# Kernel optimization log

Measured on AMD Instinct MI355X. Metric: run time of the kernel, lower is better.

Reference implementation:

```python
import jax, jax.numpy as jnp
import numpy as np
import math

DIM = 1024
WINDOW = 16
NUM_HEADS = 16
HEAD_DIM = DIM // NUM_HEADS
SCALE = math.sqrt(HEAD_DIM)
LN_EPS = 1e-5


def _gather_window(z, W):
    # z: [B, T, H, C] -> [B, T, H, W, C]; nb[:, t, :, w, :] = z[:, t-1-w] (zeros if t-1-w < 0)
    B, T, H, C = z.shape
    t = jnp.arange(T)[:, None]
    w = jnp.arange(W)[None, :]
    idx = t - 1 - w                      # [T, W]
    valid = idx >= 0
    idxc = jnp.clip(idx, 0, T - 1)
    nb = z[:, idxc]                      # [B, T, W, H, C]
    nb = jnp.where(valid[None, :, :, None, None], nb, jnp.zeros((), z.dtype))
    return nb.transpose(0, 1, 3, 2, 4)   # [B, T, H, W, C]


def setup_inputs() -> dict:
    key = jax.random.key(0)
    k0, k1, k2, k3 = jax.random.split(key, 4)
    B, T, D = 2, 4096, DIM
    x = jax.random.normal(k0, (B, T, D), dtype=jnp.float32)
    wq = jax.random.normal(k1, (D, D), dtype=jnp.float32) * 0.02
    wkv = jax.random.normal(k2, (2 * D, D), dtype=jnp.float32) * 0.02  # torch Linear weight layout [out,in]
    wo = jax.random.normal(k3, (D, D), dtype=jnp.float32) * 0.02
    gamma = jnp.ones((D,), dtype=jnp.float32)
    beta = jnp.zeros((D,), dtype=jnp.float32)
    return {"x": x, "wq": wq, "wkv": wkv, "wo": wo, "gamma": gamma, "beta": beta}


def reference(x, wq, wkv, wo, gamma, beta):
    B, T, D = x.shape
    H, HD, W = NUM_HEADS, HEAD_DIM, WINDOW
    q = (x @ wq.T).reshape(B, T, H, HD)
    kv = (x @ wkv.T).reshape(B, T, H, 2 * HD)
    nb_kv = _gather_window(kv, W)                    # [B, T, H, W, 2*HD]
    nb_k, nb_v = nb_kv[..., :HD], nb_kv[..., HD:]
    tau = jax.nn.sigmoid(jnp.einsum('bthd,bthwd->bthw', q, nb_k) / SCALE)
    msg = jnp.einsum('bthw,bthwd->bthd', tau, nb_v)  # [B, T, H, HD]
    y = x + msg.reshape(B, T, D) @ wo.T
    mu = jnp.mean(y, axis=-1, keepdims=True)
    var = jnp.mean((y - mu) ** 2, axis=-1, keepdims=True)
    out = (y - mu) * jax.lax.rsqrt(var + LN_EPS) * gamma + beta
    return out
```

## Files before the change

### kernel.cpp

```cpp
#include <hip/hip_runtime.h>
#include <hip/hip_bf16.h>

#define D_MODEL 1024
#define SEQ_T   4096
#define NBATCH  2
#define NHEADS  16
#define HEAD_D  64
#define WIN     16

typedef __attribute__((ext_vector_type(8))) short bf16x8;
typedef __attribute__((ext_vector_type(8))) unsigned short u16x8;
typedef __attribute__((ext_vector_type(4))) float f32x4;

__device__ __forceinline__ unsigned short f2bf(float f) {
  union { float f; unsigned int u; } v; v.f = f;
  unsigned int r = v.u + 0x7fffu + ((v.u >> 16) & 1u);
  return (unsigned short)(r >> 16);
}
__device__ __forceinline__ float bf2f(unsigned short u) {
  union { unsigned int u; float f; } v; v.u = ((unsigned int)u) << 16;
  return v.f;
}

#define SBAR() __builtin_amdgcn_s_barrier()
#define LGKM0() asm volatile("s_waitcnt lgkmcnt(0)" ::: "memory")
#define LGKM8() asm volatile("s_waitcnt lgkmcnt(8)" ::: "memory")
#define VMC(n) asm volatile("s_waitcnt vmcnt(" #n ")" ::: "memory")

__global__ __launch_bounds__(256) void cast_f32_bf16(const float4* __restrict__ src,
                                                     ushort* __restrict__ dst, int n4) {
  int i = blockIdx.x * 256 + threadIdx.x;
  if (i >= n4) return;
  float4 v = src[i];
  ushort4 o;
  o.x = f2bf(v.x); o.y = f2bf(v.y); o.z = f2bf(v.z); o.w = f2bf(v.w);
  *(ushort4*)(dst + (size_t)i * 4) = o;
}

__global__ __launch_bounds__(256) void cast_weights(const float4* __restrict__ wq,
                                                    const float4* __restrict__ wkv,
                                                    const float4* __restrict__ wo,
                                                    ushort* __restrict__ dst) {
  int i = blockIdx.x * 256 + threadIdx.x;
  const float4* src;
  int off;
  if (i < 262144) { src = wq; off = 0; }
  else if (i < 786432) { src = wkv; off = 262144; }
  else { src = wo; off = 786432; }
  float4 v = src[i - off];
  ushort4 o;
  o.x = f2bf(v.x); o.y = f2bf(v.y); o.z = f2bf(v.z); o.w = f2bf(v.w);
  *(ushort4*)(dst + (size_t)i * 4) = o;
}

__global__ __launch_bounds__(512, 2) void gemm1_6ph(const ushort* __restrict__ A,
                                                    const ushort* __restrict__ Bt,
                                                    ushort* __restrict__ C,
                                                    int M, int N, int K) {
  extern __shared__ char smem[];
  const int tid = threadIdx.x;
  const int wid = tid >> 6;
  const int lane = tid & 63;
  const int m0 = blockIdx.y * 256;
  const int n0 = blockIdx.x * 192;

  const int l8 = lane >> 3;
  const int lchunk = (lane & 7) ^ (l8 & 7);
  const ushort* pA = A + (size_t)(m0 + wid * 8 + l8) * K + lchunk * 8;
  const ushort* pB = Bt + (size_t)(n0 + wid * 8 + l8) * K + lchunk * 8;

#define SA(kt, db, j0)                                                                     \
  {                                                                                        \
    _Pragma("unroll") for (int j = (j0); j < (j0) + 2; ++j) {                              \
      const ushort* gp = pA + (size_t)(j * 64) * K + (size_t)(kt) * 64;                    \
      char* lp = smem + (db) * 32768 + (j * 8 + wid) * 1024;                               \
      __builtin_amdgcn_global_load_lds((const __attribute__((address_space(1))) void*)gp,  \
                                       (__attribute__((address_space(3))) void*)lp, 16, 0, 0); \
    }                                                                                      \
  }
#define SB(kt, db)                                                                         \
  {                                                                                        \
    _Pragma("unroll") for (int j = 0; j < 3; ++j) {                                        \
      const ushort* gp = pB + (size_t)(j * 64) * K + (size_t)(kt) * 64;                    \
      char* lp = smem + 65536 + (db) * 24576 + (j * 8 + wid) * 1024;                       \
      __builtin_amdgcn_global_load_lds((const __attribute__((address_space(1))) void*)gp,  \
                                       (__attribute__((address_space(3))) void*)lp, 16, 0, 0); \
    }                                                                                      \
  }

  const int fr = lane & 15;
  const int g = lane >> 4;
  const int wr = wid >> 1;
  const int wc = wid & 1;
  int aRow[4], bRow[6], ch[2];
#pragma unroll
  for (int mi = 0; mi < 4; ++mi) aRow[mi] = (wr * 64 + mi * 16 + fr) * 128;
#pragma unroll
  for (int j = 0; j < 6; ++j) bRow[j] = (wc * 96 + j * 16 + fr) * 128;
#pragma unroll
  for (int kk = 0; kk < 2; ++kk) ch[kk] = ((kk * 4 + g) ^ (fr & 7)) * 16;

  f32x4 acc[4][6];
#pragma unroll
  for (int mi = 0; mi < 4; ++mi)
#pragma unroll
    for (int j = 0; j < 6; ++j) acc[mi][j] = (f32x4){0.f, 0.f, 0.f, 0.f};

  bf16x8 a[4][2], b[2][2];

#define RD_A(db)                                                               \
  _Pragma("unroll") for (int mi = 0; mi < 4; ++mi)                             \
    _Pragma("unroll") for (int kk = 0; kk < 2; ++kk)                           \
      a[mi][kk] = *(const bf16x8*)(smem + (db) * 32768 + aRow[mi] + ch[kk]);
#define RD_B(db, nh)                                                           \
  _Pragma("unroll") for (int ni = 0; ni < 2; ++ni)                             \
    _Pragma("unroll") for (int kk = 0; kk < 2; ++kk)                           \
      b[ni][kk] = *(const bf16x8*)(smem + 65536 + (db) * 24576 +               \
                                   bRow[(nh) * 2 + ni] + ch[kk]);
#define MM(nh)                                                                 \
  __builtin_amdgcn_s_setprio(1);                                               \
  _Pragma("unroll") for (int kk = 0; kk < 2; ++kk)                             \
    _Pragma("unroll") for (int mi = 0; mi < 4; ++mi)                           \
      _Pragma("unroll") for (int ni = 0; ni < 2; ++ni)                         \
        acc[mi][(nh) * 2 + ni] = __builtin_amdgcn_mfma_f32_16x16x32_bf16(      \
            a[mi][kk], b[ni][kk], acc[mi][(nh) * 2 + ni], 0, 0, 0);            \
  __builtin_amdgcn_s_setprio(0);

  SA(0, 0, 0); SA(0, 0, 2); SB(0, 0); SA(1, 1, 0); SA(1, 1, 2);
  VMC(4);
  SBAR();

#pragma unroll 1
  for (int i = 0; i < 8; ++i) {
    const int t1 = 2 * i + 1;
    const int t2 = (2 * i + 2 < 16) ? 2 * i + 2 : 15;
    const int t3 = (2 * i + 3 < 16) ? 2 * i + 3 : 15;
    const int d2 = t2 & 1, d3 = t3 & 1;

    RD_A(0); RD_B(0, 0);
    SB(t1, 1);
    LGKM8();
    SBAR(); LGKM0();
    MM(0);
    SBAR();

    RD_B(0, 1);
    SA(t2, d2, 0);
    SBAR(); LGKM0();
    MM(1);
    SBAR();

    RD_B(0, 2);
    SA(t2, d2, 2);
    VMC(4);
    SBAR(); LGKM0();
    MM(2);
    SBAR();

    RD_A(1); RD_B(1, 0);
    SB(t2, d2);
    LGKM8();
    SBAR(); LGKM0();
    MM(0);
    SBAR();

    RD_B(1, 1);
    SA(t3, d3, 0);
    SBAR(); LGKM0();
    MM(1);
    SBAR();

    RD_B(1, 2);
    SA(t3, d3, 2);
    VMC(4);
    SBAR(); LGKM0();
    MM(2);
    SBAR();
  }

  const int cc = lane & 15;
  const int cr4 = (lane >> 4) * 4;
#pragma unroll
  for (int mi = 0; mi < 4; ++mi)
#pragma unroll
    for (int j = 0; j < 6; ++j)
#pragma unroll
      for (int r = 0; r < 4; ++r) {
        int row = m0 + wr * 64 + mi * 16 + cr4 + r;
        int col = n0 + wc * 96 + j * 16 + cc;
        C[(size_t)row * N + col] = f2bf(acc[mi][j][r]);
      }
#undef SA
#undef SB
#undef RD_A
#undef RD_B
#undef MM
}

template <int EPI>
__global__ __launch_bounds__(512, 2) void gemm_8w(const ushort* __restrict__ A,
                                                  const ushort* __restrict__ Bt,
                                                  ushort* __restrict__ Cb,
                                                  float* __restrict__ Cf,
                                                  const float* __restrict__ resid,
                                                  int M, int N, int K) {
  extern __shared__ char smem[];
  const int NTK = K >> 6;
  const int tid = threadIdx.x;
  const int wid = tid >> 6;
  const int lane = tid & 63;
  const int m0 = blockIdx.y * 256;
  const int n0 = blockIdx.x * 128;

  const int l8 = lane >> 3;
  const int lchunk = (lane & 7) ^ (l8 & 7);
  const ushort* pA = A + (size_t)(m0 + wid * 8 + l8) * K + lchunk * 8;
  const ushort* pB = Bt + (size_t)(n0 + wid * 8 + l8) * K + lchunk * 8;

#define STAGE_A(kt, db)                                                                    \
  {                                                                                        \
    _Pragma("unroll") for (int j = 0; j < 4; ++j) {                                        \
      const ushort* gp = pA + (size_t)(j * 64) * K + (size_t)(kt) * 64;                    \
      char* lp = smem + (db) * 32768 + (j * 8 + wid) * 1024;                               \
      __builtin_amdgcn_global_load_lds((const __attribute__((address_space(1))) void*)gp,  \
                                       (__attribute__((address_space(3))) void*)lp, 16, 0, 0); \
    }                                                                                      \
  }
#define STAGE_B(kt, db)                                                                    \
  {                                                                                        \
    _Pragma("unroll") for (int j = 0; j < 2; ++j) {                                        \
      const ushort* gp = pB + (size_t)(j * 64) * K + (size_t)(kt) * 64;                    \
      char* lp = smem + 65536 + (db) * 16384 + (j * 8 + wid) * 1024;                       \
      __builtin_amdgcn_global_load_lds((const __attribute__((address_space(1))) void*)gp,  \
                                       (__attribute__((address_space(3))) void*)lp, 16, 0, 0); \
    }                                                                                      \
  }

  const int fr = lane & 15;
  const int g = lane >> 4;
  const int wr = wid >> 1;
  const int wc = wid & 1;
  int aRow[4], bRow[2][2], ch[2];
#pragma unroll
  for (int mi = 0; mi < 4; ++mi) aRow[mi] = (wr * 64 + mi * 16 + fr) * 128;
#pragma unroll
  for (int nq = 0; nq < 2; ++nq)
#pragma unroll
    for (int ni = 0; ni < 2; ++ni) bRow[nq][ni] = (wc * 64 + nq * 32 + ni * 16 + fr) * 128;
#pragma unroll
  for (int kk = 0; kk < 2; ++kk) ch[kk] = ((kk * 4 + g) ^ (fr & 7)) * 16;

  f32x4 acc[2][4][2];
#pragma unroll
  for (int nq = 0; nq < 2; ++nq)
#pragma unroll
    for (int mi = 0; mi < 4; ++mi)
#pragma unroll
      for (int ni = 0; ni < 2; ++ni) acc[nq][mi][ni] = (f32x4){0.f, 0.f, 0.f, 0.f};

  bf16x8 a[4][2], b0[2][2], b1[2][2];

  STAGE_A(0, 0); STAGE_B(0, 0); STAGE_A(1, 1);
  VMC(4);
  SBAR();

#define PHASE_MFMA(nq, bfr)                                                    \
  __builtin_amdgcn_s_setprio(1);                                               \
  _Pragma("unroll") for (int kk = 0; kk < 2; ++kk)                             \
    _Pragma("unroll") for (int mi = 0; mi < 4; ++mi)                           \
      _Pragma("unroll") for (int ni = 0; ni < 2; ++ni)                         \
        acc[nq][mi][ni] = __builtin_amdgcn_mfma_f32_16x16x32_bf16(             \
            a[mi][kk], bfr[ni][kk], acc[nq][mi][ni], 0, 0, 0);                 \
  __builtin_amdgcn_s_setprio(0);

#pragma unroll 1
  for (int t = 0; t < NTK; ++t) {
    const int db = t & 1;
    const int u1 = (t + 1 < NTK) ? t + 1 : NTK - 1;
    const int u2 = (t + 2 < NTK) ? t + 2 : NTK - 1;
    const int d1 = u1 & 1, d2 = u2 & 1;
    const char* Ab = smem + db * 32768;
    const char* Bb = smem + 65536 + db * 16384;

#pragma unroll
    for (int mi = 0; mi < 4; ++mi)
#pragma unroll
      for (int kk = 0; kk < 2; ++kk)
        a[mi][kk] = *(const bf16x8*)(Ab + aRow[mi] + ch[kk]);
#pragma unroll
    for (int ni = 0; ni < 2; ++ni)
#pragma unroll
      for (int kk = 0; kk < 2; ++kk)
        b0[ni][kk] = *(const bf16x8*)(Bb + bRow[0][ni] + ch[kk]);
    STAGE_B(u1, d1);
    LGKM0();
    PHASE_MFMA(0, b0);
    VMC(2);
    SBAR();

#pragma unroll
    for (int ni = 0; ni < 2; ++ni)
#pragma unroll
      for (int kk = 0; kk < 2; ++kk)
        b1[ni][kk] = *(const bf16x8*)(Bb + bRow[1][ni] + ch[kk]);
    STAGE_A(u2, d2);
    LGKM0();
    PHASE_MFMA(1, b1);
    VMC(4);
    SBAR();
  }

  const int cc = lane & 15;
  const int cr4 = (lane >> 4) * 4;
#pragma unroll
  for (int nq = 0; nq < 2; ++nq)
#pragma unroll
    for (int mi = 0; mi < 4; ++mi)
#pragma unroll
      for (int ni = 0; ni < 2; ++ni)
#pragma unroll
        for (int r = 0; r < 4; ++r) {
          int row = m0 + wr * 64 + mi * 16 + cr4 + r;
          int col = n0 + wc * 64 + nq * 32 + ni * 16 + cc;
          size_t idx = (size_t)row * N + col;
          float v = acc[nq][mi][ni][r];
          if (EPI == 0) {
            Cb[idx] = f2bf(v);
          } else {
            Cf[idx] = v + resid[idx];
          }
        }
#undef STAGE_A
#undef STAGE_B
#undef PHASE_MFMA
}

__global__ __launch_bounds__(256) void attn_win_mfma(const ushort* __restrict__ qkv,
                                                     ushort* __restrict__ msg) {
  __shared__ ushort Ks[80][72];
  __shared__ ushort Vt[64][88];
  __shared__ ushort Ps[4][16][40];

  const int tile = blockIdx.x;
  const int h = blockIdx.y;
  const int b = blockIdx.z;
  const int t0 = tile * 64;
  const size_t rowbase = (size_t)b * SEQ_T;
  const int tid = threadIdx.x;
  const int wave = tid >> 6;
  const int lane = tid & 63;

  for (int chunk = tid; chunk < 1280; chunk += 256) {
    int r = chunk >> 4;
    int c = (chunk & 15) * 8;
    int t = t0 - 16 + r;
    u16x8 u = {0, 0, 0, 0, 0, 0, 0, 0};
    if (t >= 0)
      u = *(const u16x8*)(qkv + (rowbase + t) * 3072 + 1024 + (size_t)h * 128 + c);
    if (c < 64) {
      *(u16x8*)&Ks[r][c] = u;
    } else {
      int d0 = c - 64;
#pragma unroll
      for (int j = 0; j < 8; ++j) Vt[d0 + j][r] = u[j];
    }
  }
  __syncthreads();

  const int fr = lane & 15;
  const int g = lane >> 4;
  const int rbase = wave * 16;

  bf16x8 qa[2];
#pragma unroll
  for (int kk = 0; kk < 2; ++kk)
    qa[kk] = *(const bf16x8*)(qkv + (rowbase + t0 + wave * 16 + fr) * 3072 +
                              (size_t)h * 64 + kk * 32 + g * 8);

  f32x4 sacc[2];
  sacc[0] = (f32x4){0.f, 0.f, 0.f, 0.f};
  sacc[1] = (f32x4){0.f, 0.f, 0.f, 0.f};
#pragma unroll
  for (int kk = 0; kk < 2; ++kk) {
#pragma unroll
    for (int nt = 0; nt < 2; ++nt) {
      bf16x8 kb = *(const bf16x8*)&Ks[rbase + nt * 16 + fr][kk * 32 + g * 8];
      sacc[nt] = __builtin_amdgcn_mfma_f32_16x16x32_bf16(qa[kk], kb, sacc[nt], 0, 0, 0);
    }
  }

#pragma unroll
  for (int nt = 0; nt < 2; ++nt) {
    int tk = t0 - 16 + rbase + nt * 16 + fr;
#pragma unroll
    for (int reg = 0; reg < 4; ++reg) {
      int t = t0 + wave * 16 + g * 4 + reg;
      float tau = 0.f;
      if (tk >= 0 && tk >= t - WIN && tk <= t - 1)
        tau = 1.f / (1.f + __expf(-sacc[nt][reg] * 0.125f));
      Ps[wave][g * 4 + reg][nt * 16 + fr] = f2bf(tau);
    }
  }
  __syncthreads();

  bf16x8 pa = *(const bf16x8*)&Ps[wave][fr][g * 8];
#pragma unroll
  for (int ct = 0; ct < 4; ++ct) {
    bf16x8 vb = *(const bf16x8*)&Vt[ct * 16 + fr][rbase + g * 8];
    f32x4 m = __builtin_amdgcn_mfma_f32_16x16x32_bf16(pa, vb, (f32x4){0.f, 0.f, 0.f, 0.f}, 0, 0, 0);
#pragma unroll
    for (int reg = 0; reg < 4; ++reg) {
      int t = t0 + wave * 16 + g * 4 + reg;
      msg[(rowbase + t) * 1024 + (size_t)h * 64 + ct * 16 + fr] = f2bf(m[reg]);
    }
  }
}

__global__ __launch_bounds__(256) void layernorm_inplace(float* __restrict__ y,
                                                         const float* __restrict__ gamma,
                                                         const float* __restrict__ beta) {
  const int row = blockIdx.x;
  float* p = y + (size_t)row * D_MODEL;
  const int tid = threadIdx.x;
  float4 v = *(const float4*)&p[tid * 4];
  float s = v.x + v.y + v.z + v.w;
  float s2 = v.x * v.x + v.y * v.y + v.z * v.z + v.w * v.w;
#pragma unroll
  for (int m = 1; m < 64; m <<= 1) {
    s += __shfl_xor(s, m);
    s2 += __shfl_xor(s2, m);
  }
  __shared__ float red[8];
  const int wave = tid >> 6, lane = tid & 63;
  if (lane == 0) { red[wave] = s; red[4 + wave] = s2; }
  __syncthreads();
  s = red[0] + red[1] + red[2] + red[3];
  s2 = red[4] + red[5] + red[6] + red[7];
  const float mu = s * (1.f / D_MODEL);
  const float var = s2 * (1.f / D_MODEL) - mu * mu;
  const float rstd = rsqrtf(var + 1e-5f);
  float4 g = *(const float4*)&gamma[tid * 4];
  float4 be = *(const float4*)&beta[tid * 4];
  float4 o;
  o.x = (v.x - mu) * rstd * g.x + be.x;
  o.y = (v.y - mu) * rstd * g.y + be.y;
  o.z = (v.z - mu) * rstd * g.z + be.z;
  o.w = (v.w - mu) * rstd * g.w + be.w;
  *(float4*)&p[tid * 4] = o;
}

extern "C" void kernel_launch(void* const* d_in, const int* in_sizes, int n_in,
                              void* d_out, int out_size, void* d_ws, size_t ws_size,
                              hipStream_t stream) {
  (void)in_sizes; (void)n_in; (void)out_size; (void)ws_size;
  const float* x = (const float*)d_in[0];
  const float* wq = (const float*)d_in[1];
  const float* wkv = (const float*)d_in[2];
  const float* wo = (const float*)d_in[3];
  const float* gamma = (const float*)d_in[4];
  const float* beta = (const float*)d_in[5];
  float* out = (float*)d_out;

  ushort* xb = (ushort*)d_ws;
  ushort* wb = xb + (size_t)8192 * 1024;
  ushort* qkvb = wb + (size_t)4096 * 1024;
  ushort* msgb = qkvb + (size_t)8192 * 3072;

  const int M = NBATCH * SEQ_T;

  (void)hipFuncSetAttribute(reinterpret_cast<const void*>(&gemm1_6ph),
                            hipFuncAttributeMaxDynamicSharedMemorySize, 114688);
  (void)hipFuncSetAttribute(reinterpret_cast<const void*>(&gemm_8w<1>),
                            hipFuncAttributeMaxDynamicSharedMemorySize, 98304);

  cast_f32_bf16<<<(M * D_MODEL / 4 + 255) / 256, 256, 0, stream>>>((const float4*)x, xb, M * D_MODEL / 4);
  cast_weights<<<4096, 256, 0, stream>>>((const float4*)wq, (const float4*)wkv,
                                         (const float4*)wo, wb);

  gemm1_6ph<<<dim3(3072 / 192, M / 256), 512, 114688, stream>>>(xb, wb, qkvb, M, 3072, 1024);

  attn_win_mfma<<<dim3(SEQ_T / 64, NHEADS, NBATCH), 256, 0, stream>>>(qkvb, msgb);

  gemm_8w<1><<<dim3(1024 / 128, M / 256), 512, 98304, stream>>>(msgb, wb + (size_t)3072 * 1024,
                                                                nullptr, out, x, M, 1024, 1024);

  layernorm_inplace<<<M, 256, 0, stream>>>(out, gamma, beta);
}
```

Before: 131.5 us.

## Fuse windowed attention into QKV GEMM epilogue with per-head weight interleave

Reorders the cast weights so each 192-column GEMM tile holds one head's Q, K and V, then computes the windowed sigmoid attention directly in the GEMM epilogue from LDS. This drops the 8192x3072 QKV intermediate write and its re-read by a separate attention kernel. A small pre_kv kernel recomputes the 16 halo K/V rows preceding each 256-row tile so the fused kernel has its window context. The cost is redundant halo compute, an extra launch, and a longer epilogue with several block barriers.

After: 156.5 us. +19.0%, slower.

```diff
diff --git a/kernel.cpp b/kernel.cpp
--- a/kernel.cpp
+++ b/kernel.cpp
@@ -42,27 +42,69 @@
                                                     const float4* __restrict__ wo,
                                                     ushort* __restrict__ dst) {
   int i = blockIdx.x * 256 + threadIdx.x;
+  int n = i >> 8;
+  int k4 = i & 255;
   const float4* src;
-  int off;
-  if (i < 262144) { src = wq; off = 0; }
-  else if (i < 786432) { src = wkv; off = 262144; }
-  else { src = wo; off = 786432; }
-  float4 v = src[i - off];
+  if (n < 3072) {
+    int h = n / 192, j = n % 192;
+    if (j < 64) src = wq + ((size_t)(h * 64 + j) << 8) + k4;
+    else if (j < 128) src = wkv + ((size_t)(h * 128 + (j - 64)) << 8) + k4;
+    else src = wkv + ((size_t)(h * 128 + 64 + (j - 128)) << 8) + k4;
+  } else {
+    src = wo + ((size_t)(n - 3072) << 8) + k4;
+  }
+  float4 v = *src;
   ushort4 o;
   o.x = f2bf(v.x); o.y = f2bf(v.y); o.z = f2bf(v.z); o.w = f2bf(v.w);
   *(ushort4*)(dst + (size_t)i * 4) = o;
 }
 
-__global__ __launch_bounds__(512, 2) void gemm1_6ph(const ushort* __restrict__ A,
-                                                    const ushort* __restrict__ Bt,
-                                                    ushort* __restrict__ C,
-                                                    int M, int N, int K) {
+__global__ __launch_bounds__(256) void pre_kv(const ushort* __restrict__ xb,
+                                              const ushort* __restrict__ wb,
+                                              ushort* __restrict__ bkv) {
+  const int by = blockIdx.x;
+  const int h = blockIdx.y;
+  const int m0 = by * 256;
+  if ((m0 & (SEQ_T - 1)) == 0) return;
+  const int tid = threadIdx.x;
+  const int wv = tid >> 6;
+  const int lane = tid & 63;
+  const int fr = lane & 15, g = lane >> 4;
+
+  f32x4 acc2[2];
+  acc2[0] = (f32x4){0.f, 0.f, 0.f, 0.f};
+  acc2[1] = (f32x4){0.f, 0.f, 0.f, 0.f};
+  const ushort* arow = xb + (size_t)(m0 - 16 + fr) * 1024;
+  const ushort* b0 = wb + (size_t)(h * 192 + 64 + (wv * 2) * 16 + fr) * 1024;
+  const ushort* b1 = wb + (size_t)(h * 192 + 64 + (wv * 2 + 1) * 16 + fr) * 1024;
+#pragma unroll 4
+  for (int k0 = 0; k0 < 1024; k0 += 32) {
+    bf16x8 a = *(const bf16x8*)(arow + k0 + g * 8);
+    bf16x8 bb0 = *(const bf16x8*)(b0 + k0 + g * 8);
+    bf16x8 bb1 = *(const bf16x8*)(b1 + k0 + g * 8);
+    acc2[0] = __builtin_amdgcn_mfma_f32_16x16x32_bf16(a, bb0, acc2[0], 0, 0, 0);
+    acc2[1] = __builtin_amdgcn_mfma_f32_16x16x32_bf16(a, bb1, acc2[1], 0, 0, 0);
+  }
+#pragma unroll
+  for (int ci = 0; ci < 2; ++ci)
+#pragma unroll
+    for (int reg = 0; reg < 4; ++reg)
+      bkv[(size_t)(by * 16 + g * 4 + reg) * 2048 + h * 128 + (wv * 2 + ci) * 16 + fr] =
+          f2bf(acc2[ci][reg]);
+}
+
+__global__ __launch_bounds__(512, 2) void gemm1_fused(const ushort* __restrict__ A,
+                                                      const ushort* __restrict__ Bt,
+                                                      const ushort* __restrict__ bkv,
+                                                      ushort* __restrict__ msg,
+                                                      int M, int K) {
   extern __shared__ char smem[];
   const int tid = threadIdx.x;
   const int wid = tid >> 6;
   const int lane = tid & 63;
+  const int h = blockIdx.x;
   const int m0 = blockIdx.y * 256;
-  const int n0 = blockIdx.x * 192;
+  const int n0 = h * 192;
 
   const int l8 = lane >> 3;
   const int lchunk = (lane & 7) ^ (l8 & 7);
@@ -178,18 +220,102 @@
     SBAR();
   }
 
+  VMC(0);
+  __syncthreads();
+
+  ushort* qls = (ushort*)smem;
+  ushort* kls = (ushort*)(smem + 36864);
+  ushort* vls = (ushort*)(smem + 76032);
+  ushort* Ps = (ushort*)(smem + 95488);
+
   const int cc = lane & 15;
   const int cr4 = (lane >> 4) * 4;
-#pragma unroll
-  for (int mi = 0; mi < 4; ++mi)
-#pragma unroll
-    for (int j = 0; j < 6; ++j)
-#pragma unroll
-      for (int r = 0; r < 4; ++r) {
-        int row = m0 + wr * 64 + mi * 16 + cr4 + r;
-        int col = n0 + wc * 96 + j * 16 + cc;
-        C[(size_t)row * N + col] = f2bf(acc[mi][j][r]);
+  const int tmod = m0 & (SEQ_T - 1);
+
+#pragma unroll 1
+  for (int hf = 0; hf < 2; ++hf) {
+    const int R0 = hf * 128;
+
+#pragma unroll
+    for (int mi = 0; mi < 4; ++mi) {
+      const int lr = wr * 64 + mi * 16 + cr4;
+#pragma unroll
+      for (int j = 0; j < 6; ++j) {
+        const int cb = wc * 96 + j * 16;
+#pragma unroll
+        for (int r = 0; r < 4; ++r) {
+          const int row = lr + r;
+          const ushort hv = f2bf(acc[mi][j][r]);
+          if (cb < 64) {
+            if (row >= R0 && row < R0 + 128) qls[(row - R0) * 72 + cb + cc] = hv;
+          } else if (cb < 128) {
+            const int rr = row - R0 + 16;
+            if (rr >= 0 && rr < 144) kls[rr * 136 + (cb - 64) + cc] = hv;
+          } else {
+            const int rr = row - R0 + 16;
+            if (rr >= 0 && rr < 144) vls[((cb - 128) + cc) * 152 + rr] = hv;
+          }
+        }
       }
+    }
+    if (hf == 0 && tid < 256) {
+      const int r = tid >> 4;
+      const int c8 = (tid & 15) * 8;
+      u16x8 u = *(const u16x8*)(bkv + (size_t)(blockIdx.y * 16 + r) * 2048 + h * 128 + c8);
+      if (c8 < 64) {
+        *(u16x8*)&kls[r * 136 + c8] = u;
+      } else {
+#pragma unroll
+        for (int jj = 0; jj < 8; ++jj) vls[(c8 - 64 + jj) * 152 + r] = u[jj];
+      }
+    }
+    __syncthreads();
+
+    bf16x8 qa[2];
+#pragma unroll
+    for (int kk = 0; kk < 2; ++kk)
+      qa[kk] = *(const bf16x8*)&qls[(wid * 16 + fr) * 72 + kk * 32 + g * 8];
+
+    f32x4 sacc[2];
+    sacc[0] = (f32x4){0.f, 0.f, 0.f, 0.f};
+    sacc[1] = (f32x4){0.f, 0.f, 0.f, 0.f};
+#pragma unroll
+    for (int kk = 0; kk < 2; ++kk)
+#pragma unroll
+      for (int nt = 0; nt < 2; ++nt) {
+        bf16x8 kb = *(const bf16x8*)&kls[(wid * 16 + nt * 16 + fr) * 136 + kk * 32 + g * 8];
+        sacc[nt] = __builtin_amdgcn_mfma_f32_16x16x32_bf16(qa[kk], kb, sacc[nt], 0, 0, 0);
+      }
+
+    const int tb = tmod + R0 + wid * 16;
+#pragma unroll
+    for (int nt = 0; nt < 2; ++nt) {
+      const int kvr = nt * 16 + fr - 16;
+#pragma unroll
+      for (int reg = 0; reg < 4; ++reg) {
+        const int qr = g * 4 + reg;
+        float tau = 0.f;
+        if (kvr >= qr - WIN && kvr <= qr - 1 && tb + kvr >= 0)
+          tau = 1.f / (1.f + __expf(-sacc[nt][reg] * 0.125f));
+        Ps[wid * 640 + (g * 4 + reg) * 40 + nt * 16 + fr] = f2bf(tau);
+      }
+    }
+    __syncthreads();
+
+    bf16x8 pa = *(const bf16x8*)&Ps[wid * 640 + fr * 40 + g * 8];
+#pragma unroll
+    for (int ct = 0; ct < 4; ++ct) {
+      bf16x8 vb = *(const bf16x8*)&vls[(ct * 16 + fr) * 152 + wid * 16 + g * 8];
+      f32x4 mres = __builtin_amdgcn_mfma_f32_16x16x32_bf16(pa, vb, (f32x4){0.f, 0.f, 0.f, 0.f},
+                                                           0, 0, 0);
+#pragma unroll
+      for (int reg = 0; reg < 4; ++reg) {
+        const int row = m0 + R0 + wid * 16 + g * 4 + reg;
+        msg[(size_t)row * 1024 + h * 64 + ct * 16 + fr] = f2bf(mres[reg]);
+      }
+    }
+    __syncthreads();
+  }
 #undef SA
 #undef SB
 #undef RD_A
@@ -333,87 +459,6 @@
 #undef STAGE_A
 #undef STAGE_B
 #undef PHASE_MFMA
-}
-
-__global__ __launch_bounds__(256) void attn_win_mfma(const ushort* __restrict__ qkv,
-                                                     ushort* __restrict__ msg) {
-  __shared__ ushort Ks[80][72];
-  __shared__ ushort Vt[64][88];
-  __shared__ ushort Ps[4][16][40];
-
-  const int tile = blockIdx.x;
-  const int h = blockIdx.y;
-  const int b = blockIdx.z;
-  const int t0 = tile * 64;
-  const size_t rowbase = (size_t)b * SEQ_T;
-  const int tid = threadIdx.x;
-  const int wave = tid >> 6;
-  const int lane = tid & 63;
-
-  for (int chunk = tid; chunk < 1280; chunk += 256) {
-    int r = chunk >> 4;
-    int c = (chunk & 15) * 8;
-    int t = t0 - 16 + r;
-    u16x8 u = {0, 0, 0, 0, 0, 0, 0, 0};
-    if (t >= 0)
-      u = *(const u16x8*)(qkv + (rowbase + t) * 3072 + 1024 + (size_t)h * 128 + c);
-    if (c < 64) {
-      *(u16x8*)&Ks[r][c] = u;
-    } else {
-      int d0 = c - 64;
-#pragma unroll
-      for (int j = 0; j < 8; ++j) Vt[d0 + j][r] = u[j];
-    }
-  }
-  __syncthreads();
-
-  const int fr = lane & 15;
-  const int g = lane >> 4;
-  const int rbase = wave * 16;
-
-  bf16x8 qa[2];
-#pragma unroll
-  for (int kk = 0; kk < 2; ++kk)
-    qa[kk] = *(const bf16x8*)(qkv + (rowbase + t0 + wave * 16 + fr) * 3072 +
-                              (size_t)h * 64 + kk * 32 + g * 8);
-
-  f32x4 sacc[2];
-  sacc[0] = (f32x4){0.f, 0.f, 0.f, 0.f};
-  sacc[1] = (f32x4){0.f, 0.f, 0.f, 0.f};
-#pragma unroll
-  for (int kk = 0; kk < 2; ++kk) {
-#pragma unroll
-    for (int nt = 0; nt < 2; ++nt) {
-      bf16x8 kb = *(const bf16x8*)&Ks[rbase + nt * 16 + fr][kk * 32 + g * 8];
-      sacc[nt] = __builtin_amdgcn_mfma_f32_16x16x32_bf16(qa[kk], kb, sacc[nt], 0, 0, 0);
-    }
-  }
-
-#pragma unroll
-  for (int nt = 0; nt < 2; ++nt) {
-    int tk = t0 - 16 + rbase + nt * 16 + fr;
-#pragma unroll
-    for (int reg = 0; reg < 4; ++reg) {
-      int t = t0 + wave * 16 + g * 4 + reg;
-      float tau = 0.f;
-      if (tk >= 0 && tk >= t - WIN && tk <= t - 1)
-        tau = 1.f / (1.f + __expf(-sacc[nt][reg] * 0.125f));
-      Ps[wave][g * 4 + reg][nt * 16 + fr] = f2bf(tau);
-    }
-  }
-  __syncthreads();
-
-  bf16x8 pa = *(const bf16x8*)&Ps[wave][fr][g * 8];
-#pragma unroll
-  for (int ct = 0; ct < 4; ++ct) {
-    bf16x8 vb = *(const bf16x8*)&Vt[ct * 16 + fr][rbase + g * 8];
-    f32x4 m = __builtin_amdgcn_mfma_f32_16x16x32_bf16(pa, vb, (f32x4){0.f, 0.f, 0.f, 0.f}, 0, 0, 0);
-#pragma unroll
-    for (int reg = 0; reg < 4; ++reg) {
-      int t = t0 + wave * 16 + g * 4 + reg;
-      msg[(rowbase + t) * 1024 + (size_t)h * 64 + ct * 16 + fr] = f2bf(m[reg]);
-    }
-  }
 }
 
 __global__ __launch_bounds__(256) void layernorm_inplace(float* __restrict__ y,
@@ -463,23 +508,24 @@
 
   ushort* xb = (ushort*)d_ws;
   ushort* wb = xb + (size_t)8192 * 1024;
-  ushort* qkvb = wb + (size_t)4096 * 1024;
-  ushort* msgb = qkvb + (size_t)8192 * 3072;
+  ushort* msgb = wb + (size_t)4096 * 1024;
+  ushort* bkv = msgb + (size_t)8192 * 1024;
 
   const int M = NBATCH * SEQ_T;
 
-  (void)hipFuncSetAttribute(reinterpret_cast<const void*>(&gemm1_6ph),
+  (void)hipFuncSetAttribute(reinterpret_cast<const void*>(&gemm1_fused),
                             hipFuncAttributeMaxDynamicSharedMemorySize, 114688);
   (void)hipFuncSetAttribute(reinterpret_cast<const void*>(&gemm_8w<1>),
                             hipFuncAttributeMaxDynamicSharedMemorySize, 98304);
 
-  cast_f32_bf16<<<(M * D_MODEL / 4 + 255) / 256, 256, 0, stream>>>((const float4*)x, xb, M * D_MODEL / 4);
+  cast_f32_bf16<<<(M * D_MODEL / 4 + 255) / 256, 256, 0, stream>>>((const float4*)x, xb,
+                                                                   M * D_MODEL / 4);
   cast_weights<<<4096, 256, 0, stream>>>((const float4*)wq, (const float4*)wkv,
                                          (const float4*)wo, wb);
 
-  gemm1_6ph<<<dim3(3072 / 192, M / 256), 512, 114688, stream>>>(xb, wb, qkvb, M, 3072, 1024);
-
-  attn_win_mfma<<<dim3(SEQ_T / 64, NHEADS, NBATCH), 256, 0, stream>>>(qkvb, msgb);
+  pre_kv<<<dim3(M / 256, NHEADS), 256, 0, stream>>>(xb, wb, bkv);
+
+  gemm1_fused<<<dim3(NHEADS, M / 256), 512, 114688, stream>>>(xb, wb, bkv, msgb, M, 1024);
 
   gemm_8w<1><<<dim3(1024 / 128, M / 256), 512, 98304, stream>>>(msgb, wb + (size_t)3072 * 1024,
                                                                 nullptr, out, x, M, 1024, 1024);
```
